# Performance work log

Hardware: AMD Instinct MI355X
Metric: run time of the kernel (lower is better)

## Reference

```python
import jax, jax.numpy as jnp
import numpy as np

B, T, H = 4, 512, 768
N, S = 256, 16
NER_DIM = 32
D = H + NER_DIM  # node_in_dim = 800
L, R = 2, 15
NE, MM = 64, 8
P = 1024
E = 4096
OUT = 97
NER_NUM = 7


def setup_inputs() -> dict:
    key = jax.random.key(0)
    ks = jax.random.split(key, 20)
    f = jax.random.normal
    inp = {}
    inp['token_feature'] = f(ks[0], (B, T, H), jnp.float32)
    inp['doc_cls_feature'] = f(ks[1], (B, H), jnp.float32)
    inp['node_span_pos'] = jax.random.randint(ks[2], (B, N, S), 0, T)
    inp['node_span_mask'] = jnp.ones((B, N, S), jnp.float32)
    inp['node_ner'] = jax.random.randint(ks[3], (B, N), 0, NER_NUM + 1)
    inp['node_mask'] = jnp.ones((B, N), jnp.float32)
    inp['ent2MentionId'] = jax.random.randint(ks[4], (B, NE, MM), 0, N + 1)
    inp['ent2MentionId_mask'] = jnp.ones((B, NE, MM), jnp.float32)
    inp['ent_pair'] = jax.random.randint(ks[5], (B, P, 2), 0, NE)
    inp['edge_src'] = jax.random.randint(ks[6], (B, E), 0, N)
    inp['edge_dst'] = jax.random.randint(ks[7], (B, E), 0, N)
    inp['edge_rel'] = jax.random.randint(ks[8], (B, E), 0, R)
    inp['ment_num'] = jax.random.randint(ks[9], (B,), 0, N)
    s = lambda k, sh: f(k, sh, jnp.float32) * 0.02
    inp['nerEmb'] = s(ks[10], (NER_NUM + 1, NER_DIM))
    inp['doc_W'] = s(ks[11], (H, D))
    inp['doc_b'] = jnp.zeros((D,), jnp.float32)
    inp['W_rel'] = s(ks[12], (L, R, D, D))
    inp['W_self'] = s(ks[13], (L, D, D))
    inp['gnn_b'] = jnp.zeros((L, D), jnp.float32)
    EE = 2 * D  # entity_embed_dim = 1600
    inp['W1'] = s(ks[14], (4 * EE, 2 * EE))
    inp['b1'] = jnp.zeros((2 * EE,), jnp.float32)
    inp['W2'] = s(ks[15], (2 * EE, OUT))
    inp['b2'] = jnp.zeros((OUT,), jnp.float32)
    return inp


def reference(token_feature, doc_cls_feature, node_span_pos, node_span_mask, node_ner,
              node_mask, ent2MentionId, ent2MentionId_mask, ent_pair, edge_src,
              edge_dst, edge_rel, ment_num, nerEmb, doc_W, doc_b, W_rel, W_self,
              gnn_b, W1, b1, W2, b2):
    # span pooling: gather span tokens, masked mean (avg pool with +0.1 denom as in source)
    span_tok = jax.vmap(lambda tf, p: tf[p])(token_feature, node_span_pos)  # [B,N,S,H]
    span = (span_tok * node_span_mask[..., None]).sum(2)
    span = span / (node_span_mask.sum(2, keepdims=True) + 0.1)
    node = span + doc_cls_feature[:, None, :]  # use_doc_feature add
    doc_proj = jax.nn.relu(doc_cls_feature @ doc_W + doc_b)  # doc_feature_fc
    node = jnp.concatenate([node, nerEmb[node_ner]], -1) * node_mask[..., None]  # [B,N,D]

    def per_sample(x, docp, m, src, dst, rel, e2m, e2m_mask, pairs):
        # node_in_feature[ment_num] = doc_cls_feature
        x = x.at[m].set(docp)
        outs = []
        h = x
        for l in range(L):
            # relational graph conv: per-relation transform then gather-scatter over edges
            Hr = jnp.einsum('nd,rde->rne', h, W_rel[l])  # [R,N,D]
            msg = Hr[rel, src]                            # [E,D]
            agg = jax.ops.segment_sum(msg, dst, num_segments=N)
            h = jax.nn.relu(agg + h @ W_self[l] + gnn_b[l])
            outs.append(h)
        on = jnp.concatenate([outs[0], outs[-1]], -1)     # [N,2D]
        on = jnp.concatenate([jnp.zeros((1, on.shape[-1]), on.dtype), on], 0)  # pad row 0
        ent = (on[e2m] * e2m_mask[..., None]).sum(1) / (e2m_mask.sum(1, keepdims=True) + 1e-7)
        hf = ent[pairs[:, 0]]
        tf_ = ent[pairs[:, 1]]
        feat = jnp.concatenate([hf, tf_, jnp.abs(hf - tf_), hf * tf_], -1)  # [P,4*EE]
        return jax.nn.relu(feat @ W1 + b1) @ W2 + b2       # [P,OUT]

    return jax.vmap(per_sample)(node, doc_proj, ment_num, edge_src, edge_dst,
                                edge_rel, ent2MentionId, ent2MentionId_mask, ent_pair)
```

## Files before the change

kernel.cpp:

```cpp
#include <hip/hip_runtime.h>
#include <hip/hip_bf16.h>

#define B_    4
#define T_    512
#define H_    768
#define N_    256
#define S_    16
#define NERD  32
#define D_    800
#define L_    2
#define R_    15
#define NE_   64
#define MM_   8
#define P_    1024
#define E_    4096
#define OUT_  97
#define NW    12800
#define EE2   1600
#define KF    (4 * EE2)
#define NH    (2 * EE2)

typedef unsigned short u16;
typedef unsigned int   u32;
typedef __attribute__((ext_vector_type(8))) short  short8;
typedef __attribute__((ext_vector_type(4))) float  f32x4;

#define AS1 __attribute__((address_space(1)))
#define AS3 __attribute__((address_space(3)))

static __device__ __forceinline__ u16 f2bf(float f) {
  union { float f; u32 u; } v; v.f = f;
  u32 u = v.u;
  u32 r = (u + 0x7FFFu + ((u >> 16) & 1u)) >> 16;
  return (u16)r;
}
static __device__ __forceinline__ float bf2f(u16 h) {
  union { u32 u; float f; } v; v.u = ((u32)h) << 16;
  return v.f;
}

__global__ __launch_bounds__(256) void k_doc_proj(
    const float* __restrict__ doc_cls, const float* __restrict__ doc_W,
    const float* __restrict__ doc_b, float* __restrict__ doc_proj) {
  int i = blockIdx.x * 256 + threadIdx.x;
  if (i >= B_ * D_) return;
  int b = i / D_, d = i % D_;
  float acc = doc_b[d];
  const float* dc = doc_cls + b * H_;
#pragma unroll 4
  for (int k = 0; k < H_; k++) acc += dc[k] * doc_W[k * D_ + d];
  doc_proj[i] = fmaxf(acc, 0.f);
}

__global__ __launch_bounds__(256) void k_build_node(
    const float* __restrict__ tokf, const float* __restrict__ doc_cls,
    const int* __restrict__ span_pos, const float* __restrict__ span_mask,
    const int* __restrict__ node_ner, const float* __restrict__ node_mask,
    const int* __restrict__ ment_num, const float* __restrict__ nerEmb,
    const float* __restrict__ doc_proj, u16* __restrict__ xB) {
  int n = blockIdx.x, b = blockIdx.y;
  __shared__ int pos_s[S_];
  __shared__ float msk_s[S_];
  int tid = threadIdx.x;
  if (tid < S_) {
    pos_s[tid] = span_pos[((size_t)b * N_ + n) * S_ + tid];
    msk_s[tid] = span_mask[((size_t)b * N_ + n) * S_ + tid];
  }
  __syncthreads();
  float msum = 0.f;
#pragma unroll
  for (int s = 0; s < S_; s++) msum += msk_s[s];
  float rinv = 1.f / (msum + 0.1f);
  int m = ment_num[b];
  float nm = node_mask[b * N_ + n];
  int ner = node_ner[b * N_ + n];
  for (int d = tid; d < D_; d += 256) {
    float v;
    if (d < H_) {
      float ssum = 0.f;
#pragma unroll
      for (int s = 0; s < S_; s++)
        ssum += tokf[((size_t)b * T_ + pos_s[s]) * H_ + d] * msk_s[s];
      v = ssum * rinv + doc_cls[b * H_ + d];
    } else {
      v = nerEmb[ner * NERD + (d - H_)];
    }
    v *= nm;
    if (n == m) v = doc_proj[b * D_ + d];
    xB[((size_t)b * N_ + n) * D_ + d] = f2bf(v);
  }
}

__global__ __launch_bounds__(256) void k_wt(const float* __restrict__ W_rel,
                                            const float* __restrict__ W_self,
                                            u16* __restrict__ WT) {
  __shared__ float tile[32][33];
  int l = blockIdx.z >> 4, i = blockIdx.z & 15;
  const float* src = (i < 15) ? (W_rel + ((size_t)l * R_ + i) * D_ * D_)
                              : (W_self + (size_t)l * D_ * D_);
  u16* dst = WT + (size_t)l * NW * D_ + (size_t)i * D_ * D_;
  int d0 = blockIdx.x * 32, e0 = blockIdx.y * 32;
  int tx = threadIdx.x & 31, ty = threadIdx.x >> 5;
  for (int j = ty; j < 32; j += 8)
    tile[j][tx] = src[(size_t)(d0 + j) * D_ + e0 + tx];
  __syncthreads();
  for (int j = ty; j < 32; j += 8)
    dst[(size_t)(e0 + j) * D_ + d0 + tx] = f2bf(tile[tx][j]);
}

__global__ __launch_bounds__(256) void k_w1t(const float* __restrict__ W1,
                                             u16* __restrict__ W1T) {
  __shared__ float tile[32][33];
  int k0 = blockIdx.x * 32, n0 = blockIdx.y * 32;
  int tx = threadIdx.x & 31, ty = threadIdx.x >> 5;
  for (int i = ty; i < 32; i += 8)
    tile[i][tx] = W1[(size_t)(k0 + i) * NH + n0 + tx];
  __syncthreads();
  for (int i = ty; i < 32; i += 8)
    W1T[(size_t)(n0 + i) * KF + k0 + tx] = f2bf(tile[tx][i]);
}

__global__ __launch_bounds__(256) void k_w2t(const float* __restrict__ W2,
                                             u16* __restrict__ W2T) {
  __shared__ float tile[32][33];
  int k0 = blockIdx.x * 32, n0 = blockIdx.y * 32;
  int tx = threadIdx.x & 31, ty = threadIdx.x >> 5;
  for (int i = ty; i < 32; i += 8)
    tile[i][tx] = (n0 + tx < OUT_) ? W2[(size_t)(k0 + i) * OUT_ + n0 + tx] : 0.f;
  __syncthreads();
  for (int i = ty; i < 32; i += 8)
    W2T[(size_t)(n0 + i) * NH + k0 + tx] = f2bf(tile[tx][i]);
}

template <int KD, int EPI>
__global__ __launch_bounds__(256) void k_gemm_bt(
    const u16* __restrict__ A, int lda, const u16* __restrict__ Bm, int ldb,
    const float* __restrict__ bias, const float* __restrict__ preA,
    const float* __restrict__ preB, const int* __restrict__ pairs,
    void* __restrict__ Cv, int ldc) {
  __shared__ u16 As[128 * 32];
  __shared__ u16 Bs[128 * 32];
  int tid = threadIdx.x;
  int w = tid >> 6, lane = tid & 63;
  int wr = w >> 1, wc = w & 1;
  int lane16 = lane & 15, quad = lane >> 4;

  int nbn = gridDim.x, nbm = gridDim.y;
  int pid = blockIdx.y * nbn + blockIdx.x;
  const int GROUP = 8;
  int npg = GROUP * nbn;
  int gidg = pid / npg;
  int first = gidg * GROUP;
  int szm = min(nbm - first, GROUP);
  int pid_m = first + (pid % npg) % szm;
  int pid_n = (pid % npg) / szm;
  int n0 = pid_n * 128;
  int m0 = pid_m * 128;

  int lrow = lane >> 2;
  int lcol = (lane & 3) * 8;

  f32x4 acc[4][4] = {};

  const u16* gA = A + (size_t)m0 * lda;
  const u16* gB = Bm + (size_t)n0 * ldb;

  for (int kt = 0; kt < KD; kt += 32) {
    __syncthreads();
#pragma unroll
    for (int j = 0; j < 2; j++) {
      int chunk = j * 4 + w;
      int row = chunk * 16 + lrow;
      __builtin_amdgcn_global_load_lds(
          (const AS1 void*)(gA + (size_t)row * lda + kt + lcol),
          (AS3 void*)(As + chunk * 512 + lane * 8), 16, 0, 0);
      __builtin_amdgcn_global_load_lds(
          (const AS1 void*)(gB + (size_t)row * ldb + kt + lcol),
          (AS3 void*)(Bs + chunk * 512 + lane * 8), 16, 0, 0);
    }
    __syncthreads();

    short8 af[4], bf[4];
#pragma unroll
    for (int mi = 0; mi < 4; mi++) {
      int ml = wr * 64 + mi * 16 + lane16;
      af[mi] = *(const short8*)(As + ml * 32 + quad * 8);
    }
#pragma unroll
    for (int ni = 0; ni < 4; ni++) {
      int nl = wc * 64 + ni * 16 + lane16;
      bf[ni] = *(const short8*)(Bs + nl * 32 + quad * 8);
    }
#pragma unroll
    for (int mi = 0; mi < 4; mi++)
#pragma unroll
      for (int ni = 0; ni < 4; ni++)
        acc[mi][ni] = __builtin_amdgcn_mfma_f32_16x16x32_bf16(
            af[mi], bf[ni], acc[mi][ni], 0, 0, 0);
  }

  int cols[4];
  float bv[4];
#pragma unroll
  for (int ni = 0; ni < 4; ni++) {
    cols[ni] = n0 + wc * 64 + ni * 16 + lane16;
    if (EPI == 2) bv[ni] = bias[cols[ni]];
    if (EPI == 3) bv[ni] = (cols[ni] < OUT_) ? bias[cols[ni]] : 0.f;
  }
#pragma unroll
  for (int mi = 0; mi < 4; mi++) {
#pragma unroll
    for (int r = 0; r < 4; r++) {
      int row = m0 + wr * 64 + mi * 16 + quad * 4 + r;
      const float* pAr = nullptr;
      const float* pBr = nullptr;
      if (EPI == 2) {
        int hp = pairs[2 * row], tp = pairs[2 * row + 1];
        int pb = (row >> 10) * NE_;
        pAr = preA + (size_t)(pb + hp) * NH;
        pBr = preB + (size_t)(pb + tp) * NH;
      }
#pragma unroll
      for (int ni = 0; ni < 4; ni++) {
        float v = acc[mi][ni][r];
        int col = cols[ni];
        if (EPI == 0) {
          ((u16*)Cv)[(size_t)row * ldc + col] = f2bf(v);
        } else if (EPI == 1) {
          ((float*)Cv)[(size_t)row * ldc + col] = v;
        } else if (EPI == 2) {
          v += bv[ni] + pAr[col] + pBr[col];
          ((u16*)Cv)[(size_t)row * ldc + col] = f2bf(fmaxf(v, 0.f));
        } else {
          if (col < OUT_)
            ((float*)Cv)[(size_t)row * ldc + col] = v + bv[ni];
        }
      }
    }
  }
}

__global__ __launch_bounds__(256) void k_agg(
    const u16* __restrict__ Hr, const int* __restrict__ esrc,
    const int* __restrict__ edst, const int* __restrict__ erel,
    const float* __restrict__ gnn_b, int layer,
    float* __restrict__ hout, u16* __restrict__ houtB) {
  int n = blockIdx.x, b = blockIdx.y;
  __shared__ int s_pk[E_];
  __shared__ int s_cnt;
  int tid = threadIdx.x;
  if (tid == 0) s_cnt = 0;
  __syncthreads();
  const int* dstp = edst + (size_t)b * E_;
  const int* srcp = esrc + (size_t)b * E_;
  const int* relp = erel + (size_t)b * E_;
  for (int e = tid; e < E_; e += 256) {
    if (dstp[e] == n) {
      int i = atomicAdd(&s_cnt, 1);
      s_pk[i] = srcp[e] | (relp[e] << 9);
    }
  }
  __syncthreads();
  int cnt = s_cnt;
  const u16* HrB = Hr + (size_t)b * N_ * NW;
  for (int c = tid; c < D_; c += 256) {
    float acc = bf2f(HrB[(size_t)n * NW + R_ * D_ + c]) + gnn_b[layer * D_ + c];
    for (int i = 0; i < cnt; i++) {
      int pk = s_pk[i];
      acc += bf2f(HrB[(size_t)(pk & 511) * NW + (pk >> 9) * D_ + c]);
    }
    float r = fmaxf(acc, 0.f);
    hout[((size_t)b * N_ + n) * D_ + c] = r;
    houtB[((size_t)b * N_ + n) * D_ + c] = f2bf(r);
  }
}

__global__ __launch_bounds__(256) void k_ent(
    const float* __restrict__ h0, const float* __restrict__ h1,
    const int* __restrict__ e2m, const float* __restrict__ e2m_mask,
    float* __restrict__ ent, u16* __restrict__ entB) {
  int e = blockIdx.x, b = blockIdx.y;
  __shared__ int idx_s[MM_];
  __shared__ float msk_s[MM_];
  int tid = threadIdx.x;
  if (tid < MM_) {
    idx_s[tid] = e2m[((size_t)b * NE_ + e) * MM_ + tid];
    msk_s[tid] = e2m_mask[((size_t)b * NE_ + e) * MM_ + tid];
  }
  __syncthreads();
  float msum = 0.f;
#pragma unroll
  for (int m = 0; m < MM_; m++) msum += msk_s[m];
  float inv = 1.f / (msum + 1e-7f);
  for (int c = tid; c < EE2; c += 256) {
    const float* base = (c < D_) ? h0 : h1;
    int cc = (c < D_) ? c : c - D_;
    float s = 0.f;
#pragma unroll
    for (int m = 0; m < MM_; m++) {
      int j = idx_s[m];
      if (j > 0) s += base[((size_t)b * N_ + (j - 1)) * D_ + cc] * msk_s[m];
    }
    float v = s * inv;
    ent[((size_t)b * NE_ + e) * EE2 + c] = v;
    entB[((size_t)b * NE_ + e) * EE2 + c] = f2bf(v);
  }
}

__global__ __launch_bounds__(256) void k_featC(
    const float* __restrict__ ent, const int* __restrict__ ent_pair,
    u16* __restrict__ featC) {
  int row = blockIdx.x;
  int b = row >> 10, g = row & 1023;
  int hp = ent_pair[(((size_t)b << 10) + g) * 2 + 0];
  int tp = ent_pair[(((size_t)b << 10) + g) * 2 + 1];
  const float* eh = ent + ((size_t)b * NE_ + hp) * EE2;
  const float* et = ent + ((size_t)b * NE_ + tp) * EE2;
  u16* orow = featC + (size_t)row * NH;
  for (int c = threadIdx.x; c < 800; c += 256) {
    int seg = c / 400, kk = (c - seg * 400) * 4;
    float4 hf = *(const float4*)(eh + kk);
    float4 tf = *(const float4*)(et + kk);
    float4 v;
    if (seg == 0) {
      v.x = fabsf(hf.x - tf.x); v.y = fabsf(hf.y - tf.y);
      v.z = fabsf(hf.z - tf.z); v.w = fabsf(hf.w - tf.w);
    } else {
      v.x = hf.x * tf.x; v.y = hf.y * tf.y;
      v.z = hf.z * tf.z; v.w = hf.w * tf.w;
    }
    ushort4 o;
    o.x = f2bf(v.x); o.y = f2bf(v.y); o.z = f2bf(v.z); o.w = f2bf(v.w);
    *(ushort4*)(orow + seg * EE2 + kk) = o;
  }
}

extern "C" void kernel_launch(void* const* d_in, const int* in_sizes, int n_in,
                              void* d_out, int out_size, void* d_ws, size_t ws_size,
                              hipStream_t stream) {
  const float* token_feature = (const float*)d_in[0];
  const float* doc_cls       = (const float*)d_in[1];
  const int*   span_pos      = (const int*)d_in[2];
  const float* span_mask     = (const float*)d_in[3];
  const int*   node_ner      = (const int*)d_in[4];
  const float* node_mask     = (const float*)d_in[5];
  const int*   e2m           = (const int*)d_in[6];
  const float* e2m_mask      = (const float*)d_in[7];
  const int*   ent_pair      = (const int*)d_in[8];
  const int*   edge_src      = (const int*)d_in[9];
  const int*   edge_dst      = (const int*)d_in[10];
  const int*   edge_rel      = (const int*)d_in[11];
  const int*   ment_num      = (const int*)d_in[12];
  const float* nerEmb        = (const float*)d_in[13];
  const float* doc_W         = (const float*)d_in[14];
  const float* doc_b         = (const float*)d_in[15];
  const float* W_rel         = (const float*)d_in[16];
  const float* W_self        = (const float*)d_in[17];
  const float* gnn_b         = (const float*)d_in[18];
  const float* W1            = (const float*)d_in[19];
  const float* b1            = (const float*)d_in[20];
  const float* W2            = (const float*)d_in[21];
  const float* b2            = (const float*)d_in[22];
  float* out = (float*)d_out;

  float* ws = (float*)d_ws;
  size_t off = 0;
  auto alloc = [&](size_t n) {
    float* p = ws + off;
    off += (n + 63) & ~size_t(63);
    return p;
  };
  float* doc_proj = alloc(B_ * D_);
  u16*   xB  = (u16*)alloc((size_t)B_ * N_ * D_ / 2);
  float* h0  = alloc((size_t)B_ * N_ * D_);
  float* h1  = alloc((size_t)B_ * N_ * D_);
  u16*   hB  = (u16*)alloc((size_t)B_ * N_ * D_ / 2);
  float* ent = alloc((size_t)B_ * NE_ * EE2);
  u16*   entB = (u16*)alloc((size_t)B_ * NE_ * EE2 / 2);
  u16*   WT  = (u16*)alloc((size_t)L_ * NW * D_ / 2);
  u16*   W1T = (u16*)alloc((size_t)NH * KF / 2);
  u16*   W2T = (u16*)alloc((size_t)128 * NH / 2);
  float* preA = alloc((size_t)B_ * NE_ * NH);
  float* preB = alloc((size_t)B_ * NE_ * NH);
  u16*   Hr    = (u16*)alloc((size_t)B_ * N_ * NW / 2);
  u16*   featC = Hr;
  u16*   hiddenB = (u16*)alloc((size_t)B_ * P_ * NH / 2);
  (void)ws_size;

  k_wt<<<dim3(D_ / 32, D_ / 32, L_ * 16), 256, 0, stream>>>(W_rel, W_self, WT);
  k_w1t<<<dim3(KF / 32, NH / 32), 256, 0, stream>>>(W1, W1T);
  k_w2t<<<dim3(NH / 32, 4), 256, 0, stream>>>(W2, W2T);

  k_doc_proj<<<dim3((B_ * D_ + 255) / 256), 256, 0, stream>>>(doc_cls, doc_W, doc_b, doc_proj);
  k_build_node<<<dim3(N_, B_), 256, 0, stream>>>(token_feature, doc_cls, span_pos, span_mask,
                                                 node_ner, node_mask, ment_num, nerEmb,
                                                 doc_proj, xB);
  const u16* hin = xB;
  float* houts[2] = {h0, h1};
  for (int l = 0; l < L_; l++) {
    k_gemm_bt<D_, 0><<<dim3(NW / 128, (B_ * N_) / 128), 256, 0, stream>>>(
        hin, D_, WT + (size_t)l * NW * D_, D_, nullptr, nullptr, nullptr, nullptr,
        Hr, NW);
    k_agg<<<dim3(N_, B_), 256, 0, stream>>>(Hr, edge_src, edge_dst, edge_rel,
                                            gnn_b, l, houts[l], hB);
    hin = hB;
  }
  k_ent<<<dim3(NE_, B_), 256, 0, stream>>>(h0, h1, e2m, e2m_mask, ent, entB);

  k_gemm_bt<EE2, 1><<<dim3(NH / 128, (B_ * NE_) / 128), 256, 0, stream>>>(
      entB, EE2, W1T, KF, nullptr, nullptr, nullptr, nullptr, preA, NH);
  k_gemm_bt<EE2, 1><<<dim3(NH / 128, (B_ * NE_) / 128), 256, 0, stream>>>(
      entB, EE2, W1T + EE2, KF, nullptr, nullptr, nullptr, nullptr, preB, NH);

  k_featC<<<dim3(B_ * P_), 256, 0, stream>>>(ent, ent_pair, featC);

  k_gemm_bt<NH, 2><<<dim3(NH / 128, (B_ * P_) / 128), 256, 0, stream>>>(
      featC, NH, W1T + 2 * EE2, KF, b1, preA, preB, ent_pair, hiddenB, NH);

  k_gemm_bt<NH, 3><<<dim3(1, (B_ * P_) / 128), 256, 0, stream>>>(
      hiddenB, NH, W2T, NH, b2, nullptr, nullptr, nullptr, out, OUT_);
}
```

Measured before the change: 829.6 us.

## Build CSR edge lists, merge pre-projection GEMMs, split-K the output GEMM

```diff
diff --git a/kernel.cpp b/kernel.cpp
--- a/kernel.cpp
+++ b/kernel.cpp
@@ -19,6 +19,8 @@
 #define EE2   1600
 #define KF    (4 * EE2)
 #define NH    (2 * EE2)
+#define KS    800
+#define NZ    4
 
 typedef unsigned short u16;
 typedef unsigned int   u32;
@@ -109,15 +111,21 @@
 }
 
 __global__ __launch_bounds__(256) void k_w1t(const float* __restrict__ W1,
-                                             u16* __restrict__ W1T) {
+                                             u16* __restrict__ W1abT,
+                                             u16* __restrict__ W1cdT) {
   __shared__ float tile[32][33];
   int k0 = blockIdx.x * 32, n0 = blockIdx.y * 32;
   int tx = threadIdx.x & 31, ty = threadIdx.x >> 5;
   for (int i = ty; i < 32; i += 8)
     tile[i][tx] = W1[(size_t)(k0 + i) * NH + n0 + tx];
   __syncthreads();
-  for (int i = ty; i < 32; i += 8)
-    W1T[(size_t)(n0 + i) * KF + k0 + tx] = f2bf(tile[tx][i]);
+  for (int i = ty; i < 32; i += 8) {
+    int kk = k0 + tx, n = n0 + i;
+    u16 v = f2bf(tile[tx][i]);
+    if (kk < EE2)            W1abT[(size_t)n * EE2 + kk] = v;
+    else if (kk < 2 * EE2)   W1abT[(size_t)(NH + n) * EE2 + (kk - EE2)] = v;
+    else                     W1cdT[(size_t)n * NH + (kk - 2 * EE2)] = v;
+  }
 }
 
 __global__ __launch_bounds__(256) void k_w2t(const float* __restrict__ W2,
@@ -132,12 +140,49 @@
     W2T[(size_t)(n0 + i) * NH + k0 + tx] = f2bf(tile[tx][i]);
 }
 
+__global__ __launch_bounds__(256) void k_csr_zero(int* __restrict__ cnt) {
+  cnt[blockIdx.x * 256 + threadIdx.x] = 0;
+}
+__global__ __launch_bounds__(256) void k_csr_count(const int* __restrict__ edst,
+                                                   int* __restrict__ cnt) {
+  int e = blockIdx.x * 256 + threadIdx.x, b = blockIdx.y;
+  atomicAdd(&cnt[b * N_ + edst[(size_t)b * E_ + e]], 1);
+}
+__global__ __launch_bounds__(256) void k_csr_scan(const int* __restrict__ cnt,
+                                                  int* __restrict__ rowptr,
+                                                  int* __restrict__ cursor) {
+  int b = blockIdx.x, t = threadIdx.x;
+  __shared__ int s[N_];
+  int own = cnt[b * N_ + t];
+  s[t] = own;
+  __syncthreads();
+  for (int off = 1; off < N_; off <<= 1) {
+    int v = (t >= off) ? s[t - off] : 0;
+    __syncthreads();
+    s[t] += v;
+    __syncthreads();
+  }
+  int excl = s[t] - own;
+  rowptr[b * (N_ + 1) + t] = excl;
+  cursor[b * N_ + t] = excl;
+  if (t == 0) rowptr[b * (N_ + 1) + N_] = E_;
+}
+__global__ __launch_bounds__(256) void k_csr_fill(
+    const int* __restrict__ esrc, const int* __restrict__ edst,
+    const int* __restrict__ erel, int* __restrict__ cursor,
+    int* __restrict__ elist) {
+  int e = blockIdx.x * 256 + threadIdx.x, b = blockIdx.y;
+  size_t ei = (size_t)b * E_ + e;
+  int pos = atomicAdd(&cursor[b * N_ + edst[ei]], 1);
+  elist[b * E_ + pos] = esrc[ei] | (erel[ei] << 9);
+}
+
 template <int KD, int EPI>
 __global__ __launch_bounds__(256) void k_gemm_bt(
     const u16* __restrict__ A, int lda, const u16* __restrict__ Bm, int ldb,
     const float* __restrict__ bias, const float* __restrict__ preA,
     const float* __restrict__ preB, const int* __restrict__ pairs,
-    void* __restrict__ Cv, int ldc) {
+    void* __restrict__ Cv, int ldc, int ldpre, long long zA, long long zC) {
   __shared__ u16 As[128 * 32];
   __shared__ u16 Bs[128 * 32];
   int tid = threadIdx.x;
@@ -162,8 +207,8 @@
 
   f32x4 acc[4][4] = {};
 
-  const u16* gA = A + (size_t)m0 * lda;
-  const u16* gB = Bm + (size_t)n0 * ldb;
+  const u16* gA = A + (size_t)blockIdx.z * zA + (size_t)m0 * lda;
+  const u16* gB = Bm + (size_t)blockIdx.z * zA + (size_t)n0 * ldb;
 
   for (int kt = 0; kt < KD; kt += 32) {
     __syncthreads();
@@ -204,9 +249,9 @@
 #pragma unroll
   for (int ni = 0; ni < 4; ni++) {
     cols[ni] = n0 + wc * 64 + ni * 16 + lane16;
-    if (EPI == 2) bv[ni] = bias[cols[ni]];
-    if (EPI == 3) bv[ni] = (cols[ni] < OUT_) ? bias[cols[ni]] : 0.f;
-  }
+    if (EPI == 4) bv[ni] = (cols[ni] < NH) ? bias[cols[ni]] : 0.f;
+  }
+  float* Cf = (float*)Cv + (size_t)blockIdx.z * zC;
 #pragma unroll
   for (int mi = 0; mi < 4; mi++) {
 #pragma unroll
@@ -217,8 +262,8 @@
       if (EPI == 2) {
         int hp = pairs[2 * row], tp = pairs[2 * row + 1];
         int pb = (row >> 10) * NE_;
-        pAr = preA + (size_t)(pb + hp) * NH;
-        pBr = preB + (size_t)(pb + tp) * NH;
+        pAr = preA + (size_t)(pb + hp) * ldpre;
+        pBr = preB + (size_t)(pb + tp) * ldpre;
       }
 #pragma unroll
       for (int ni = 0; ni < 4; ni++) {
@@ -227,46 +272,43 @@
         if (EPI == 0) {
           ((u16*)Cv)[(size_t)row * ldc + col] = f2bf(v);
         } else if (EPI == 1) {
-          ((float*)Cv)[(size_t)row * ldc + col] = v;
+          Cf[(size_t)row * ldc + col] = v;
         } else if (EPI == 2) {
-          v += bv[ni] + pAr[col] + pBr[col];
+          v += pAr[col] + pBr[col];
           ((u16*)Cv)[(size_t)row * ldc + col] = f2bf(fmaxf(v, 0.f));
-        } else {
-          if (col < OUT_)
-            ((float*)Cv)[(size_t)row * ldc + col] = v + bv[ni];
+        } else if (EPI == 4) {
+          Cf[(size_t)row * ldc + col] = v + bv[ni];
         }
       }
     }
   }
 }
 
+__global__ __launch_bounds__(128) void k_out_reduce(
+    const float* __restrict__ part, const float* __restrict__ b2,
+    float* __restrict__ out) {
+  int row = blockIdx.x, c = threadIdx.x;
+  if (c >= OUT_) return;
+  float s = b2[c];
+#pragma unroll
+  for (int z = 0; z < NZ; z++)
+    s += part[(size_t)z * (B_ * P_ * 128) + (size_t)row * 128 + c];
+  out[(size_t)row * OUT_ + c] = s;
+}
+
 __global__ __launch_bounds__(256) void k_agg(
-    const u16* __restrict__ Hr, const int* __restrict__ esrc,
-    const int* __restrict__ edst, const int* __restrict__ erel,
-    const float* __restrict__ gnn_b, int layer,
+    const u16* __restrict__ Hr, const int* __restrict__ rowptr,
+    const int* __restrict__ elist, const float* __restrict__ gnn_b, int layer,
     float* __restrict__ hout, u16* __restrict__ houtB) {
   int n = blockIdx.x, b = blockIdx.y;
-  __shared__ int s_pk[E_];
-  __shared__ int s_cnt;
+  int beg = rowptr[b * (N_ + 1) + n], end = rowptr[b * (N_ + 1) + n + 1];
+  const int* el = elist + (size_t)b * E_;
+  const u16* HrB = Hr + (size_t)b * N_ * NW;
   int tid = threadIdx.x;
-  if (tid == 0) s_cnt = 0;
-  __syncthreads();
-  const int* dstp = edst + (size_t)b * E_;
-  const int* srcp = esrc + (size_t)b * E_;
-  const int* relp = erel + (size_t)b * E_;
-  for (int e = tid; e < E_; e += 256) {
-    if (dstp[e] == n) {
-      int i = atomicAdd(&s_cnt, 1);
-      s_pk[i] = srcp[e] | (relp[e] << 9);
-    }
-  }
-  __syncthreads();
-  int cnt = s_cnt;
-  const u16* HrB = Hr + (size_t)b * N_ * NW;
   for (int c = tid; c < D_; c += 256) {
     float acc = bf2f(HrB[(size_t)n * NW + R_ * D_ + c]) + gnn_b[layer * D_ + c];
-    for (int i = 0; i < cnt; i++) {
-      int pk = s_pk[i];
+    for (int i = beg; i < end; i++) {
+      int pk = el[i];
       acc += bf2f(HrB[(size_t)(pk & 511) * NW + (pk >> 9) * D_ + c]);
     }
     float r = fmaxf(acc, 0.f);
@@ -377,18 +419,29 @@
   u16*   hB  = (u16*)alloc((size_t)B_ * N_ * D_ / 2);
   float* ent = alloc((size_t)B_ * NE_ * EE2);
   u16*   entB = (u16*)alloc((size_t)B_ * NE_ * EE2 / 2);
-  u16*   WT  = (u16*)alloc((size_t)L_ * NW * D_ / 2);
-  u16*   W1T = (u16*)alloc((size_t)NH * KF / 2);
-  u16*   W2T = (u16*)alloc((size_t)128 * NH / 2);
-  float* preA = alloc((size_t)B_ * NE_ * NH);
-  float* preB = alloc((size_t)B_ * NE_ * NH);
+  u16*   WT    = (u16*)alloc((size_t)L_ * NW * D_ / 2);
+  u16*   W1abT = (u16*)alloc((size_t)KF * EE2 / 2);
+  u16*   W1cdT = (u16*)alloc((size_t)NH * NH / 2);
+  u16*   W2T   = (u16*)alloc((size_t)128 * NH / 2);
+  float* preAB = alloc((size_t)B_ * NE_ * KF);
   u16*   Hr    = (u16*)alloc((size_t)B_ * N_ * NW / 2);
   u16*   featC = Hr;
   u16*   hiddenB = (u16*)alloc((size_t)B_ * P_ * NH / 2);
+  float* part    = alloc((size_t)NZ * B_ * P_ * 128);
+  int*   csr_cnt    = (int*)alloc(B_ * N_ / 1 * sizeof(int) / 4);
+  int*   csr_rowptr = (int*)alloc(B_ * (N_ + 1));
+  int*   csr_cursor = (int*)alloc(B_ * N_);
+  int*   csr_elist  = (int*)alloc(B_ * E_);
   (void)ws_size;
 
+  k_csr_zero<<<dim3(B_), 256, 0, stream>>>(csr_cnt);
+  k_csr_count<<<dim3(E_ / 256, B_), 256, 0, stream>>>(edge_dst, csr_cnt);
+  k_csr_scan<<<dim3(B_), 256, 0, stream>>>(csr_cnt, csr_rowptr, csr_cursor);
+  k_csr_fill<<<dim3(E_ / 256, B_), 256, 0, stream>>>(edge_src, edge_dst, edge_rel,
+                                                     csr_cursor, csr_elist);
+
   k_wt<<<dim3(D_ / 32, D_ / 32, L_ * 16), 256, 0, stream>>>(W_rel, W_self, WT);
-  k_w1t<<<dim3(KF / 32, NH / 32), 256, 0, stream>>>(W1, W1T);
+  k_w1t<<<dim3(KF / 32, NH / 32), 256, 0, stream>>>(W1, W1abT, W1cdT);
   k_w2t<<<dim3(NH / 32, 4), 256, 0, stream>>>(W2, W2T);
 
   k_doc_proj<<<dim3((B_ * D_ + 255) / 256), 256, 0, stream>>>(doc_cls, doc_W, doc_b, doc_proj);
@@ -400,23 +453,24 @@
   for (int l = 0; l < L_; l++) {
     k_gemm_bt<D_, 0><<<dim3(NW / 128, (B_ * N_) / 128), 256, 0, stream>>>(
         hin, D_, WT + (size_t)l * NW * D_, D_, nullptr, nullptr, nullptr, nullptr,
-        Hr, NW);
-    k_agg<<<dim3(N_, B_), 256, 0, stream>>>(Hr, edge_src, edge_dst, edge_rel,
+        Hr, NW, 0, 0, 0);
+    k_agg<<<dim3(N_, B_), 256, 0, stream>>>(Hr, csr_rowptr, csr_elist,
                                             gnn_b, l, houts[l], hB);
     hin = hB;
   }
   k_ent<<<dim3(NE_, B_), 256, 0, stream>>>(h0, h1, e2m, e2m_mask, ent, entB);
 
-  k_gemm_bt<EE2, 1><<<dim3(NH / 128, (B_ * NE_) / 128), 256, 0, stream>>>(
-      entB, EE2, W1T, KF, nullptr, nullptr, nullptr, nullptr, preA, NH);
-  k_gemm_bt<EE2, 1><<<dim3(NH / 128, (B_ * NE_) / 128), 256, 0, stream>>>(
-      entB, EE2, W1T + EE2, KF, nullptr, nullptr, nullptr, nullptr, preB, NH);
+  k_gemm_bt<EE2, 4><<<dim3(KF / 128, (B_ * NE_) / 128), 256, 0, stream>>>(
+      entB, EE2, W1abT, EE2, b1, nullptr, nullptr, nullptr, preAB, KF, 0, 0, 0);
 
   k_featC<<<dim3(B_ * P_), 256, 0, stream>>>(ent, ent_pair, featC);
 
   k_gemm_bt<NH, 2><<<dim3(NH / 128, (B_ * P_) / 128), 256, 0, stream>>>(
-      featC, NH, W1T + 2 * EE2, KF, b1, preA, preB, ent_pair, hiddenB, NH);
-
-  k_gemm_bt<NH, 3><<<dim3(1, (B_ * P_) / 128), 256, 0, stream>>>(
-      hiddenB, NH, W2T, NH, b2, nullptr, nullptr, nullptr, out, OUT_);
-}
+      featC, NH, W1cdT, NH, nullptr, preAB, preAB + NH, ent_pair, hiddenB, NH,
+      KF, 0, 0);
+
+  k_gemm_bt<KS, 1><<<dim3(1, (B_ * P_) / 128, NZ), 256, 0, stream>>>(
+      hiddenB, NH, W2T, NH, nullptr, nullptr, nullptr, nullptr, part, 128,
+      0, KS, (long long)B_ * P_ * 128);
+  k_out_reduce<<<dim3(B_ * P_), 128, 0, stream>>>(part, b2, out);
+}
```

Result: faster. 783.9 us (-5.5%).
